# Kernel tuning notes

Hardware: AMD Instinct MI355X
Metric: run time of the kernel (lower is better)

Reference implementation:

```python
import jax, jax.numpy as jnp
import numpy as np

H, W = 1080, 1920
NPART = 25          # BODY_25 joint parts (channel 25 is background)
NLIMB = 26          # 26 PAF limbs -> 52 PAF channels
K = 32              # max peaks kept per joint (static top-k)
MID = 10            # mid_num line samples
THRE1 = 0.1
SIGMA = 3.0
RADIUS = 12         # scipy gaussian_filter: int(truncate*sigma+0.5), truncate=4
# BODY_25 limb sequence (SKEL25DEF.paf_dict), paired with mapIdx [[2k,2k+1]]
LIMBS = np.array([[1,8],[1,2],[1,5],[2,3],[3,4],[5,6],[6,7],[8,9],[9,10],
                  [10,11],[8,12],[12,13],[13,14],[1,0],[0,15],[15,16],[0,17],
                  [0,18],[14,19],[19,20],[14,21],[11,22],[22,23],[11,24],
                  [2,17],[5,18]], dtype=np.int32)


def gaussian_blur(x):
    """Separable gaussian filter, sigma=3, scipy mode='reflect' (= np symmetric). x: [H,W,C]."""
    C = x.shape[-1]
    t = jnp.arange(-RADIUS, RADIUS + 1, dtype=x.dtype)
    k = jnp.exp(-0.5 * (t / SIGMA) ** 2)
    k = k / k.sum()
    dn = ('NHWC', 'HWIO', 'NHWC')
    # vertical pass
    xp = jnp.pad(x, ((RADIUS, RADIUS), (0, 0), (0, 0)), mode='symmetric')[None]
    kh = jnp.tile(k.reshape(-1, 1, 1, 1), (1, 1, 1, C))
    x1 = jax.lax.conv_general_dilated(xp, kh, (1, 1), 'VALID',
                                      dimension_numbers=dn, feature_group_count=C)
    # horizontal pass
    x1 = jnp.pad(x1, ((0, 0), (0, 0), (RADIUS, RADIUS), (0, 0)), mode='symmetric')
    kw = jnp.tile(k.reshape(1, -1, 1, 1), (1, 1, 1, C))
    x2 = jax.lax.conv_general_dilated(x1, kw, (1, 1), 'VALID',
                                      dimension_numbers=dn, feature_group_count=C)
    return x2[0]


def openpose_post(heatmap_avg, paf_avg):
    maps = heatmap_avg[:, :, :NPART]                      # [H,W,25] map_ori per part
    sm = gaussian_blur(maps)                              # one_heatmap per part
    z_row = jnp.zeros((1, W, NPART), sm.dtype)
    z_col = jnp.zeros((H, 1, NPART), sm.dtype)
    m_left = jnp.concatenate([z_row, sm[:-1]], axis=0)
    m_right = jnp.concatenate([sm[1:], z_row], axis=0)
    m_up = jnp.concatenate([z_col, sm[:, :-1]], axis=1)
    m_down = jnp.concatenate([sm[:, 1:], z_col], axis=1)
    peaks_bin = ((sm >= m_left) & (sm >= m_right) & (sm >= m_up)
                 & (sm >= m_down) & (sm > THRE1))
    # static per-part top-K peaks, scored by the ORIGINAL (unblurred) map value
    flat = jnp.where(peaks_bin, maps, -1e9).transpose(2, 0, 1).reshape(NPART, H * W)
    vals, idx = jax.lax.top_k(flat, K)                    # [25,K]
    mask = vals > -1e8
    py = (idx // W).astype(jnp.int32)
    px = (idx % W).astype(jnp.int32)
    peak_x = px.astype(maps.dtype)
    peak_y = py.astype(maps.dtype)
    peak_scores = jnp.where(mask, vals, 0.0)

    limbs = jnp.asarray(LIMBS)
    ax, ay, ma = peak_x[limbs[:, 0]], peak_y[limbs[:, 0]], mask[limbs[:, 0]]  # [26,K]
    bx, by, mb = peak_x[limbs[:, 1]], peak_y[limbs[:, 1]], mask[limbs[:, 1]]
    paf_pairs = jnp.moveaxis(paf_avg.reshape(H, W, NLIMB, 2), 2, 0)           # [26,H,W,2]

    def limb_conn(paf2, ax, ay, bx, by, ma, mb):
        vx = bx[None, :] - ax[:, None]                    # [K,K]
        vy = by[None, :] - ay[:, None]
        norm = jnp.sqrt(vx * vx + vy * vy) + 1e-10
        ux, uy = vx / norm, vy / norm
        t = jnp.linspace(0.0, 1.0, MID, dtype=ax.dtype)   # matches np.linspace(a,b,10)
        sx = jnp.round(ax[:, None, None] + vx[:, :, None] * t).astype(jnp.int32)  # [K,K,MID]
        sy = jnp.round(ay[:, None, None] + vy[:, :, None] * t).astype(jnp.int32)
        pvx = paf2[sy, sx, 0]
        pvy = paf2[sy, sx, 1]
        score = (pvx * ux[:, :, None] + pvy * uy[:, :, None]).mean(-1)
        score = jnp.clip(score, 0.0, 1.0)
        return jnp.where(ma[:, None] & mb[None, :], score, 0.0)

    conn = jax.vmap(limb_conn)(paf_pairs, ax, ay, bx, by, ma, mb)             # [26,K,K]
    return peak_x, peak_y, peak_scores, mask, conn


def setup_inputs() -> dict:
    key = jax.random.key(0)
    k1, k2 = jax.random.split(key)
    heatmap_avg = jax.random.uniform(k1, (H, W, NPART + 1), dtype=jnp.float32)
    paf_avg = jax.random.normal(k2, (H, W, 2 * NLIMB), dtype=jnp.float32) * 0.3
    return {"heatmap_avg": heatmap_avg, "paf_avg": paf_avg}


def reference(heatmap_avg, paf_avg):
    return openpose_post(heatmap_avg, paf_avg)
```

## Files before the change

### kernel.cpp

```cpp
#include <hip/hip_runtime.h>
#include <math.h>
#include <float.h>

#define H 1080
#define W 1920
#define HWSZ (H*W)
#define NPART 25
#define NCH 26
#define NLIMB 26
#define KTOP 32
#define MID 10
#define RAD 12

#define EPS1 4e-6f
#define EPS2 1.5e-7
#define BLCAP (1 << 20)
#define B3CAP 65536
#define NS 16

#define VB 10
#define VXT 16
#define VCHUNK 50
#define TH2 14
#define TW2B 256
#define VTC2 282
#define VTS2 283
#define SMS2 257

#define OFF_PY   800
#define OFF_SC   1600
#define OFF_MK   2400
#define OFF_CONN 3200

__device__ __constant__ int LIMBS_d[NLIMB * 2] = {
    1,8, 1,2, 1,5, 2,3, 3,4, 5,6, 6,7, 8,9, 9,10, 10,11, 8,12, 12,13, 13,14,
    1,0, 0,15, 15,16, 0,17, 0,18, 14,19, 19,20, 14,21, 11,22, 22,23, 11,24, 2,17, 5,18
};

__device__ __forceinline__ int symH(int y) {
    if (y < 0) return -1 - y;
    if (y >= H) return 2 * H - 1 - y;
    return y;
}
__device__ __forceinline__ int symW(int x) {
    if (x < 0) return -1 - x;
    if (x >= W) return 2 * W - 1 - x;
    return x;
}

__global__ void winit_k(double* __restrict__ gw64, float* __restrict__ gw32)
{
    if (threadIdx.x == 0) {
        double wd[25]; double s = 0.0;
        for (int t = 0; t < 25; ++t) {
            double u = (double)(t - 12) / 3.0;
            wd[t] = exp(-0.5 * u * u); s += wd[t];
        }
        for (int t = 0; t < 13; ++t) {
            double w = wd[t] / s;
            gw64[t] = w;
            gw32[t] = (float)w;
        }
    }
}

__global__ __launch_bounds__(416) void vert_k(
    const float* __restrict__ hm, float* __restrict__ vpl,
    const double* __restrict__ gw64)
{
    __shared__ float ldv[VB][26][17];
    const int tid = threadIdx.x;
    const int x0 = blockIdx.x * VXT;
    const int ys = blockIdx.y * VCHUNK;
    const int c  = tid % 26;
    const int xo = tid / 26;
    const int gx = x0 + xo;

    double ws[13];
    #pragma unroll
    for (int t = 0; t < 13; ++t) ws[t] = gw64[t];

    const size_t cstr = (size_t)W * NCH;
    const size_t base = (size_t)gx * NCH + c;
    const bool yint = (ys >= 12) && (ys + 61 < H);

    double win[25];
    if (yint) {
        const float* p0 = hm + (size_t)(ys - 12) * cstr + base;
        #pragma unroll
        for (int k = 0; k < 24; ++k) { win[k] = (double)*p0; p0 += cstr; }
    } else {
        #pragma unroll
        for (int k = 0; k < 24; ++k) {
            int ry = symH(ys - 12 + k);
            win[k] = (double)hm[(size_t)ry * cstr + base];
        }
    }
    win[24] = 0.0;

    const float* pn = hm + (size_t)symH(ys + 12) * cstr + base;

    #pragma unroll 1
    for (int blk = 0; blk < VCHUNK; blk += 25) {
        #pragma unroll
        for (int p = 0; p < 25; ++p) {
            const int yo = blk + p;
            const int y  = ys + yo;
            double nv;
            if (yint) { nv = (double)*pn; pn += cstr; }
            else      { int ry = symH(y + 12); nv = (double)hm[(size_t)ry * cstr + base]; }
            win[(p + 24) % 25] = nv;
            double acc = 0.0;
            #pragma unroll
            for (int t = 0; t < 25; ++t)
                acc = fma(ws[t < 13 ? t : 24 - t], win[(p + t) % 25], acc);
            if (c < 25) ldv[yo % VB][c][xo] = (float)acc;
            if ((yo % VB) == VB - 1) {
                __syncthreads();
                const int c2 = tid >> 4, x2 = tid & 15;
                if (c2 < 25) {
                    const int yb = ys + yo - (VB - 1);
                    #pragma unroll
                    for (int i = 0; i < VB; ++i) {
                        int yr = yb + i;
                        if (yr < H)
                            vpl[(size_t)c2 * HWSZ + (size_t)yr * W + x0 + x2] = ldv[i][c2][x2];
                    }
                }
                __syncthreads();
            }
        }
    }
}

__global__ __launch_bounds__(256) void horiz_nms_k(
    const float* __restrict__ vpl, const float* __restrict__ hm,
    float* __restrict__ cval, int* __restrict__ cidx,
    int* __restrict__ counters, unsigned int* __restrict__ blg,
    const float* __restrict__ gw32, int cap)
{
    __shared__ __align__(16) float ubuf[16 * VTS2];
    float (*vt)[VTS2]  = reinterpret_cast<float(*)[VTS2]>(ubuf);
    float (*smt)[SMS2] = reinterpret_cast<float(*)[SMS2]>(ubuf);
    __shared__ unsigned short cand[TH2 * TW2B];
    __shared__ unsigned int bl[1024];
    __shared__ int lcount, bcount, gbase, gbase2;

    const int tid = threadIdx.x;
    const int r   = tid & 15;
    const int g   = tid >> 4;
    const int ch  = blockIdx.z;
    const int x0  = blockIdx.x * TW2B;
    const int y0  = blockIdx.y * TH2;
    const float* vp = vpl + (size_t)ch * HWSZ;

    if (tid == 0) { lcount = 0; bcount = 0; }
    float w32[13];
    #pragma unroll
    for (int t = 0; t < 13; ++t) w32[t] = gw32[t];

    {
        const int lr  = tid >> 4;
        const int lc0 = tid & 15;
        int gy = y0 - 1 + lr;
        gy = gy < 0 ? 0 : (gy >= H ? H - 1 : gy);
        const float* rowp = vp + (size_t)gy * W;
        const bool xint = (x0 >= 13) && (x0 + (VTC2 - 13) <= W);
        if (xint) {
            const float* p = rowp + (x0 - 13) + lc0;
            #pragma unroll
            for (int j = 0; j < 18; ++j) {
                int cc = lc0 + 16 * j;
                if (cc < VTC2) vt[lr][cc] = p[16 * j];
            }
        } else {
            #pragma unroll
            for (int j = 0; j < 18; ++j) {
                int cc = lc0 + 16 * j;
                if (cc < VTC2) vt[lr][cc] = rowp[symW(x0 - 13 + cc)];
            }
        }
    }
    __syncthreads();

    float xr[42];
    {
        const float* vrow = &vt[r][g * 16];
        #pragma unroll
        for (int t = 0; t < 42; ++t) xr[t] = vrow[t];
    }
    __syncthreads();

    float a[18];
    #pragma unroll
    for (int k = 0; k < 18; ++k) a[k] = 0.f;
    #pragma unroll
    for (int tap = 0; tap < 25; ++tap) {
        const int wi = tap < 13 ? tap : 24 - tap;
        const float wt = w32[wi];
        #pragma unroll
        for (int k = 0; k < 18; ++k)
            a[k] = fmaf(wt, xr[k + tap], a[k]);
    }

    const int gy_r = y0 - 1 + r;
    {
        const bool rowok = (gy_r >= 0 && gy_r < H);
        #pragma unroll
        for (int k = 1; k <= 16; ++k) {
            int j = g * 16 + k - 1;
            int gxj = x0 + j;
            smt[r][j] = (rowok && gxj < W) ? a[k] : 0.f;
        }
    }
    __syncthreads();

    if (r >= 1 && r <= 14 && gy_r < H) {
        const float* up = &smt[r - 1][g * 16];
        const float* dn = &smt[r + 1][g * 16];
        const int ly = r - 1;
        #pragma unroll
        for (int k = 0; k < 16; ++k) {
            int gx = x0 + g * 16 + k;
            if (gx >= W) continue;
            float s  = a[k + 1];
            float lv = (gx == 0) ? 0.f : a[k];
            float rv = (gx + 1 >= W) ? 0.f : a[k + 2];
            float dT = s - 0.1f;
            float d0 = s - up[k];
            float d1 = s - dn[k];
            float d2 = s - lv;
            float d3 = s - rv;
            int flags = (fabsf(dT) <= EPS1 ? 1 : 0)
                      | (fabsf(d0) <= EPS1 ? 2 : 0)
                      | (fabsf(d1) <= EPS1 ? 4 : 0)
                      | (fabsf(d2) <= EPS1 ? 8 : 0)
                      | (fabsf(d3) <= EPS1 ? 16 : 0);
            if (!flags) {
                if (dT > 0.f && d0 >= 0.f && d1 >= 0.f && d2 >= 0.f && d3 >= 0.f) {
                    int pos = atomicAdd(&lcount, 1);
                    cand[pos] = (unsigned short)((ly << 8) | (g * 16 + k));
                }
            } else {
                bool fail = (!(flags & 1)  && dT <= 0.f) ||
                            (!(flags & 2)  && d0 <  0.f) ||
                            (!(flags & 4)  && d1 <  0.f) ||
                            (!(flags & 8)  && d2 <  0.f) ||
                            (!(flags & 16) && d3 <  0.f);
                if (!fail) {
                    unsigned int ent = ((unsigned int)ch << 26) | ((unsigned int)flags << 21)
                                     | (unsigned int)((y0 + ly) * W + gx);
                    int bp = atomicAdd(&bcount, 1);
                    if (bp < 1024) bl[bp] = ent;
                    else {
                        int gp = atomicAdd(&counters[32], 1);
                        if (gp < BLCAP) blg[gp] = ent;
                    }
                }
            }
        }
    }
    __syncthreads();

    if (tid == 0) {
        gbase  = atomicAdd(&counters[ch], lcount);
        int nb = bcount < 1024 ? bcount : 1024;
        gbase2 = atomicAdd(&counters[32], nb);
    }
    __syncthreads();
    int n = lcount, b = gbase;
    for (int i = tid; i < n; i += 256) {
        int p = b + i;
        if (p < cap) {
            int e = cand[i];
            int ly = e >> 8, lx = e & 255;
            int gpix = (y0 + ly) * W + (x0 + lx);
            cval[(size_t)ch * cap + p] = hm[(size_t)gpix * NCH + ch];
            cidx[(size_t)ch * cap + p] = gpix;
        }
    }
    int nb = bcount < 1024 ? bcount : 1024;
    for (int i = tid; i < nb; i += 256) {
        int gp = gbase2 + i;
        if (gp < BLCAP) blg[gp] = bl[i];
    }
}

__device__ __forceinline__ double smh2(const float* __restrict__ vp,
                                       const double* w64s, int y, int x)
{
    int lane = threadIdx.x & 63;
    double term = 0.0;
    if (lane < 25) {
        int cx = symW(x - RAD + lane);
        int wi = lane < 13 ? lane : 24 - lane;
        term = w64s[wi] * (double)vp[(size_t)y * W + cx];
    }
    #pragma unroll
    for (int off = 16; off > 0; off >>= 1)
        term += __shfl_xor(term, off, 64);
    return __shfl(term, 0, 64);
}

__global__ __launch_bounds__(64) void recheck2_k(
    const float* __restrict__ vpl, const float* __restrict__ hm,
    float* __restrict__ cval, int* __restrict__ cidx,
    int* __restrict__ counters, const unsigned int* __restrict__ blg,
    unsigned int* __restrict__ bl3, const double* __restrict__ gw64, int cap)
{
    __shared__ double w64s[13];
    const int tid = threadIdx.x;
    if (tid < 13) w64s[tid] = gw64[tid];
    __syncthreads();

    int total = counters[32];
    if (total > BLCAP) total = BLCAP;
    for (int e = blockIdx.x; e < total; e += gridDim.x) {
        unsigned int ent = blg[e];
        int ch    = (int)(ent >> 26);
        int flags = (int)((ent >> 21) & 31);
        int gpix  = (int)(ent & 0x1FFFFFu);
        int gy = gpix / W, gx = gpix - gy * W;
        const float* vp = vpl + (size_t)ch * HWSZ;

        double sc = smh2(vp, w64s, gy, gx);
        bool dead = false; bool esc = false;
        if (flags & 1) {
            double d = sc - 0.1;
            if (d <= -EPS2) dead = true; else if (d < EPS2) esc = true;
        }
        if (!dead && (flags & 2)) {
            double nv = (gy - 1 >= 0) ? smh2(vp, w64s, gy - 1, gx) : 0.0;
            double d = sc - nv;
            if (d <= -EPS2) dead = true; else if (d < EPS2) esc = true;
        }
        if (!dead && (flags & 4)) {
            double nv = (gy + 1 < H) ? smh2(vp, w64s, gy + 1, gx) : 0.0;
            double d = sc - nv;
            if (d <= -EPS2) dead = true; else if (d < EPS2) esc = true;
        }
        if (!dead && (flags & 8)) {
            double nv = (gx - 1 >= 0) ? smh2(vp, w64s, gy, gx - 1) : 0.0;
            double d = sc - nv;
            if (d <= -EPS2) dead = true; else if (d < EPS2) esc = true;
        }
        if (!dead && (flags & 16)) {
            double nv = (gx + 1 < W) ? smh2(vp, w64s, gy, gx + 1) : 0.0;
            double d = sc - nv;
            if (d <= -EPS2) dead = true; else if (d < EPS2) esc = true;
        }
        if (!dead && tid == 0) {
            if (esc) {
                int p = atomicAdd(&counters[33], 1);
                if (p < B3CAP) bl3[p] = ent;
            } else {
                int p = atomicAdd(&counters[ch], 1);
                if (p < cap) {
                    cval[(size_t)ch * cap + p] = hm[(size_t)gpix * NCH + ch];
                    cidx[(size_t)ch * cap + p] = gpix;
                }
            }
        }
    }
}

__device__ double sm64_eval(const float* __restrict__ hm, int ch,
                            const double* w64s, int y, int x)
{
    int lane = threadIdx.x & 63;
    double colsum = 0.0;
    if (lane < 25) {
        int cx = symW(x - RAD + lane);
        float xv[25];
        #pragma unroll
        for (int t = 0; t < 25; t++) {
            int ry = symH(y - RAD + t);
            xv[t] = hm[((size_t)ry * W + cx) * NCH + ch];
        }
        #pragma unroll
        for (int t = 0; t < 25; t++)
            colsum = fma(w64s[t < 13 ? t : 24 - t], (double)xv[t], colsum);
    }
    double acc = 0.0;
    for (int ci = 0; ci < 25; ci++) {
        double cs = __shfl(colsum, ci, 64);
        acc = fma(w64s[ci < 13 ? ci : 24 - ci], cs, acc);
    }
    return acc;
}

__global__ __launch_bounds__(64) void recheck3_k(
    const float* __restrict__ hm,
    float* __restrict__ cval, int* __restrict__ cidx,
    int* __restrict__ counters, const unsigned int* __restrict__ bl3,
    const double* __restrict__ gw64, int cap)
{
    __shared__ double w64s[13];
    const int tid = threadIdx.x;
    if (tid < 13) w64s[tid] = gw64[tid];
    __syncthreads();

    int total = counters[33];
    if (total > B3CAP) total = B3CAP;
    for (int e = blockIdx.x; e < total; e += gridDim.x) {
        unsigned int ent = bl3[e];
        int ch    = (int)(ent >> 26);
        int flags = (int)((ent >> 21) & 31);
        int gpix  = (int)(ent & 0x1FFFFFu);
        int gy = gpix / W, gx = gpix - gy * W;
        double sc = sm64_eval(hm, ch, w64s, gy, gx);
        bool ok = (flags & 1) ? (sc > 0.1) : true;
        if (ok && (flags & 2))  { double nv = (gy - 1 >= 0) ? sm64_eval(hm, ch, w64s, gy - 1, gx) : 0.0; ok = (sc >= nv); }
        if (ok && (flags & 4))  { double nv = (gy + 1 <  H) ? sm64_eval(hm, ch, w64s, gy + 1, gx) : 0.0; ok = (sc >= nv); }
        if (ok && (flags & 8))  { double nv = (gx - 1 >= 0) ? sm64_eval(hm, ch, w64s, gy, gx - 1) : 0.0; ok = (sc >= nv); }
        if (ok && (flags & 16)) { double nv = (gx + 1 <  W) ? sm64_eval(hm, ch, w64s, gy, gx + 1) : 0.0; ok = (sc >= nv); }
        if (tid == 0 && ok) {
            int p = atomicAdd(&counters[ch], 1);
            if (p < cap) {
                cval[(size_t)ch * cap + p] = hm[(size_t)gpix * NCH + ch];
                cidx[(size_t)ch * cap + p] = gpix;
            }
        }
    }
}

#define TH 32
#define TW 64
#define LR (TH + 2*RAD + 2)
#define LC 90
#define VRR 34
#define VC (TW + 2*RAD + 2)
#define SR 34
#define SC 66
__global__ __launch_bounds__(256) void blur_peaks_gather(
    const float* __restrict__ hm,
    float* __restrict__ cval, int* __restrict__ cidx,
    int* __restrict__ counters, int cap)
{
    __shared__ float  in_t[LR][LC];
    __shared__ double v[VRR][VC];
    __shared__ double smv[SR][SC];
    __shared__ double wgt[2 * RAD + 1];
    __shared__ double wsum;

    const int tid = threadIdx.x;
    const int ch  = blockIdx.x;
    const int x0  = blockIdx.y * TW;
    const int y0  = blockIdx.z * TH;

    if (tid < 2 * RAD + 1) {
        double t = (double)(tid - RAD) / 3.0;
        wgt[tid] = exp(-0.5 * t * t);
    }
    __syncthreads();
    if (tid == 0) {
        double s = 0.0;
        for (int i = 0; i < 2 * RAD + 1; i++) s += wgt[i];
        wsum = s;
    }
    __syncthreads();
    if (tid < 2 * RAD + 1) wgt[tid] /= wsum;

    for (int i = tid; i < LR * LC; i += 256) {
        int r = i / LC, c = i % LC;
        int gy = symH(y0 - RAD - 1 + r);
        int gx = symW(x0 - RAD - 1 + c);
        in_t[r][c] = hm[((size_t)gy * W + gx) * NCH + ch];
    }
    __syncthreads();

    for (int i = tid; i < VRR * VC; i += 256) {
        int r = i / VC, c = i % VC;
        double acc = 0.0;
        #pragma unroll
        for (int t = 0; t < 2 * RAD + 1; t++)
            acc = fma(wgt[t], (double)in_t[r + t][c], acc);
        v[r][c] = acc;
    }
    __syncthreads();

    for (int i = tid; i < SR * SC; i += 256) {
        int r = i / SC, cc = i % SC;
        int gy = y0 - 1 + r;
        int gx = x0 - 1 + cc;
        double acc = 0.0;
        if (gy >= 0 && gy < H && gx >= 0 && gx < W) {
            #pragma unroll
            for (int t = 0; t < 2 * RAD + 1; t++)
                acc = fma(wgt[t], v[r][cc + t], acc);
        }
        smv[r][cc] = acc;
    }
    __syncthreads();

    for (int i = tid; i < TH * TW; i += 256) {
        int ly = i / TW, lx = i % TW;
        int gy = y0 + ly, gx = x0 + lx;
        if (gy >= H || gx >= W) continue;
        double s = smv[ly + 1][lx + 1];
        if (s > 0.1 &&
            s >= smv[ly][lx + 1] && s >= smv[ly + 2][lx + 1] &&
            s >= smv[ly + 1][lx] && s >= smv[ly + 1][lx + 2]) {
            float val = in_t[ly + RAD + 1][lx + RAD + 1];
            int pos = atomicAdd(&counters[ch], 1);
            if (pos < cap) {
                cval[(size_t)ch * cap + pos] = val;
                cidx[(size_t)ch * cap + pos] = gy * W + gx;
            }
        }
    }
}

#define BT 128
__global__ __launch_bounds__(BT) void topk1_kernel(
    const float* __restrict__ cval, const int* __restrict__ cidx,
    const int* __restrict__ counters, int cap,
    unsigned long long* __restrict__ s1)
{
    __shared__ unsigned long long lk[KTOP * BT];
    __shared__ unsigned long long rk[BT];
    __shared__ int rw[BT];
    __shared__ int winner;

    const int tid = threadIdx.x;
    const int sl  = blockIdx.x;
    const int ch  = blockIdx.y;
    int n = counters[ch];
    if (n > cap) n = cap;

    int cnt = 0;
    for (int j = sl * BT + tid; j < n; j += NS * BT) {
        float v = cval[(size_t)ch * cap + j];
        unsigned int u = __float_as_uint(v);
        u = (u & 0x80000000u) ? ~u : (u | 0x80000000u);
        unsigned long long key =
            ((unsigned long long)u << 32) |
            (unsigned int)(0xFFFFFFFFu - (unsigned int)cidx[(size_t)ch * cap + j]);
        if (cnt == KTOP) {
            if (key <= lk[(KTOP - 1) * BT + tid]) continue;
            cnt = KTOP - 1;
        }
        int i = cnt;
        while (i > 0 && key > lk[(i - 1) * BT + tid]) {
            lk[i * BT + tid] = lk[(i - 1) * BT + tid];
            i--;
        }
        lk[i * BT + tid] = key;
        cnt++;
    }
    int cur = 0;
    __syncthreads();

    for (int k = 0; k < KTOP; k++) {
        rk[tid] = (cur < cnt) ? lk[cur * BT + tid] : 0ULL;
        rw[tid] = tid;
        __syncthreads();
        for (int s = BT / 2; s > 0; s >>= 1) {
            if (tid < s) {
                if (rk[tid + s] > rk[tid]) { rk[tid] = rk[tid + s]; rw[tid] = rw[tid + s]; }
            }
            __syncthreads();
        }
        if (tid == 0) {
            winner = rw[0];
            s1[((size_t)ch * NS + sl) * KTOP + k] = rk[0];
        }
        __syncthreads();
        if (tid == winner && cur < cnt) cur++;
        __syncthreads();
    }
}

__global__ __launch_bounds__(BT) void topk2_kernel(
    const unsigned long long* __restrict__ s1,
    const int* __restrict__ counters, int cap, float* __restrict__ out)
{
    __shared__ unsigned long long sk[NS * KTOP];
    const int tid = threadIdx.x;
    const int ch  = blockIdx.x;

    for (int i = tid; i < NS * KTOP; i += BT)
        sk[i] = s1[(size_t)ch * NS * KTOP + i];
    __syncthreads();

    for (int k = 2; k <= NS * KTOP; k <<= 1) {
        for (int j = k >> 1; j > 0; j >>= 1) {
            for (int t = tid; t < NS * KTOP; t += BT) {
                int ixj = t ^ j;
                if (ixj > t) {
                    unsigned long long a = sk[t], b = sk[ixj];
                    bool sw = ((t & k) == 0) ? (a < b) : (a > b);
                    if (sw) { sk[t] = b; sk[ixj] = a; }
                }
            }
            __syncthreads();
        }
    }

    int n = counters[ch];
    if (n > cap) n = cap;
    if (tid < KTOP) {
        unsigned long long bk = sk[tid];
        float px, py, sc, mk;
        if (bk == 0ULL) {
            int fake = tid - n; if (fake < 0) fake = 0;
            px = (float)(fake % W); py = (float)(fake / W); sc = 0.f; mk = 0.f;
        } else {
            unsigned int u = (unsigned int)(bk >> 32);
            unsigned int fb = (u & 0x80000000u) ? (u ^ 0x80000000u) : ~u;
            float v = __uint_as_float(fb);
            int idx = (int)(0xFFFFFFFFu - (unsigned int)(bk & 0xFFFFFFFFu));
            px = (float)(idx % W); py = (float)(idx / W); sc = v; mk = 1.f;
        }
        out[ch * KTOP + tid]          = px;
        out[OFF_PY + ch * KTOP + tid] = py;
        out[OFF_SC + ch * KTOP + tid] = sc;
        out[OFF_MK + ch * KTOP + tid] = mk;
    }
}

__global__ __launch_bounds__(BT) void topk_kernel(
    const float* __restrict__ cval, const int* __restrict__ cidx,
    const int* __restrict__ counters, int cap, float* __restrict__ out)
{
    __shared__ unsigned long long lk[KTOP * BT];
    __shared__ unsigned long long rk[BT];
    __shared__ int rw[BT];
    __shared__ int winner;

    const int tid = threadIdx.x;
    const int ch  = blockIdx.x;
    int n = counters[ch];
    if (n > cap) n = cap;

    int cnt = 0;
    for (int j = tid; j < n; j += BT) {
        float v = cval[(size_t)ch * cap + j];
        unsigned int u = __float_as_uint(v);
        u = (u & 0x80000000u) ? ~u : (u | 0x80000000u);
        unsigned long long key =
            ((unsigned long long)u << 32) |
            (unsigned int)(0xFFFFFFFFu - (unsigned int)cidx[(size_t)ch * cap + j]);
        if (cnt == KTOP) {
            if (key <= lk[(KTOP - 1) * BT + tid]) continue;
            cnt = KTOP - 1;
        }
        int i = cnt;
        while (i > 0 && key > lk[(i - 1) * BT + tid]) {
            lk[i * BT + tid] = lk[(i - 1) * BT + tid];
            i--;
        }
        lk[i * BT + tid] = key;
        cnt++;
    }
    int cur = 0;
    __syncthreads();

    for (int k = 0; k < KTOP; k++) {
        rk[tid] = (cur < cnt) ? lk[cur * BT + tid] : 0ULL;
        rw[tid] = tid;
        __syncthreads();
        for (int s = BT / 2; s > 0; s >>= 1) {
            if (tid < s) {
                if (rk[tid + s] > rk[tid]) { rk[tid] = rk[tid + s]; rw[tid] = rw[tid + s]; }
            }
            __syncthreads();
        }
        if (tid == 0) {
            winner = rw[0];
            unsigned long long bk = rk[0];
            float px, py, sc, mk;
            if (bk == 0ULL) {
                int fake = k - n; if (fake < 0) fake = 0;
                px = (float)(fake % W); py = (float)(fake / W); sc = 0.f; mk = 0.f;
            } else {
                unsigned int u = (unsigned int)(bk >> 32);
                unsigned int fb = (u & 0x80000000u) ? (u ^ 0x80000000u) : ~u;
                float v = __uint_as_float(fb);
                int idx = (int)(0xFFFFFFFFu - (unsigned int)(bk & 0xFFFFFFFFu));
                px = (float)(idx % W); py = (float)(idx / W); sc = v; mk = 1.f;
            }
            out[ch * KTOP + k]          = px;
            out[OFF_PY + ch * KTOP + k] = py;
            out[OFF_SC + ch * KTOP + k] = sc;
            out[OFF_MK + ch * KTOP + k] = mk;
        }
        __syncthreads();
        if (tid == winner && cur < cnt) cur++;
        __syncthreads();
    }
}

__global__ __launch_bounds__(1024) void limbs_kernel(
    const float* __restrict__ pk, const float* __restrict__ paf,
    float* __restrict__ out)
{
    const int l = blockIdx.x;
    const int tid = threadIdx.x;
    const int i = tid >> 5;
    const int j = tid & 31;
    const int A = LIMBS_d[2 * l], B = LIMBS_d[2 * l + 1];

    float ax = pk[A * KTOP + i],          ay = pk[OFF_PY + A * KTOP + i];
    float ma = pk[OFF_MK + A * KTOP + i];
    float bx = pk[B * KTOP + j],          by = pk[OFF_PY + B * KTOP + j];
    float mb = pk[OFF_MK + B * KTOP + j];

    float vx = bx - ax, vy = by - ay;
    float norm = sqrtf(vx * vx + vy * vy) + 1e-10f;
    float ux = vx / norm, uy = vy / norm;

    const float step = 1.0f / 9.0f;
    float sum = 0.f;
    #pragma unroll
    for (int m = 0; m < MID; m++) {
        float t = (float)m * step;
        int sx = (int)rintf(ax + vx * t);
        int sy = (int)rintf(ay + vy * t);
        const float* p = paf + ((size_t)sy * W + sx) * (2 * NLIMB) + 2 * l;
        sum += p[0] * ux + p[1] * uy;
    }
    float score = sum / (float)MID;
    score = score < 0.f ? 0.f : (score > 1.f ? 1.f : score);
    float res = (ma != 0.f && mb != 0.f) ? score : 0.f;
    out[OFF_CONN + l * (KTOP * KTOP) + i * KTOP + j] = res;
}

extern "C" void kernel_launch(void* const* d_in, const int* in_sizes, int n_in,
                              void* d_out, int out_size, void* d_ws, size_t ws_size,
                              hipStream_t stream)
{
    const float* hm  = (const float*)d_in[0];
    const float* paf = (const float*)d_in[1];
    float* out = (float*)d_out;

    const size_t vpl_bytes = (size_t)NPART * HWSZ * sizeof(float);
    const size_t bl_bytes  = (size_t)BLCAP * 4;
    const size_t b3_bytes  = (size_t)B3CAP * 4;
    const size_t s1_bytes  = (size_t)NPART * NS * KTOP * 8;
    const size_t head = 512;

    bool pathA = false;
    int cap = 1;
    if (ws_size > head + vpl_bytes + bl_bytes + b3_bytes + s1_bytes
                 + (size_t)NPART * 8 * 4096 + 1024) {
        size_t avail = ws_size - head - vpl_bytes - bl_bytes - b3_bytes - s1_bytes - 1024;
        long long c = (long long)(avail / ((size_t)NPART * 8));
        cap = c > 65536 ? 65536 : (int)c;
        pathA = true;
    } else {
        size_t avail = ws_size > head ? ws_size - head : 0;
        long long c = (long long)(avail / ((size_t)NPART * 8));
        cap = c > 65536 ? 65536 : (int)c;
        if (cap < 1) cap = 1;
    }

    int*    counters = (int*)d_ws;
    double* gw64 = (double*)((char*)d_ws + 256);
    float*  gw32 = (float*)((char*)d_ws + 384);
    float* cval = (float*)((char*)d_ws + head);
    int*   cidx = (int*)(cval + (size_t)NPART * cap);
    unsigned long long* s1 = (unsigned long long*)(cidx + (size_t)NPART * cap);
    unsigned int* blg = (unsigned int*)(s1 + (pathA ? (size_t)NPART * NS * KTOP : 0));
    unsigned int* bl3 = blg + (pathA ? (size_t)BLCAP : 0);
    float* vpl = (float*)(bl3 + (pathA ? (size_t)B3CAP : 0));
    vpl = (float*)(((uintptr_t)vpl + 255) & ~(uintptr_t)255);

    hipMemsetAsync(d_ws, 0, 256, stream);

    if (pathA) {
        winit_k<<<1, 64, 0, stream>>>(gw64, gw32);
        dim3 g1(W / VXT, (H + VCHUNK - 1) / VCHUNK);
        vert_k<<<g1, 416, 0, stream>>>(hm, vpl, gw64);
        dim3 g2((W + TW2B - 1) / TW2B, (H + TH2 - 1) / TH2, NPART);
        horiz_nms_k<<<g2, 256, 0, stream>>>(vpl, hm, cval, cidx, counters, blg, gw32, cap);
        recheck2_k<<<2048, 64, 0, stream>>>(vpl, hm, cval, cidx, counters, blg, bl3, gw64, cap);
        recheck3_k<<<256, 64, 0, stream>>>(hm, cval, cidx, counters, bl3, gw64, cap);
        dim3 gt(NS, NPART);
        topk1_kernel<<<gt, BT, 0, stream>>>(cval, cidx, counters, cap, s1);
        topk2_kernel<<<NPART, BT, 0, stream>>>(s1, counters, cap, out);
    } else {
        dim3 gA(NPART, (W + TW - 1) / TW, (H + TH - 1) / TH);
        blur_peaks_gather<<<gA, 256, 0, stream>>>(hm, cval, cidx, counters, cap);
        topk_kernel<<<NPART, BT, 0, stream>>>(cval, cidx, counters, cap, out);
    }
    limbs_kernel<<<NLIMB, 1024, 0, stream>>>(out, paf, out);
}
```

Baseline: 534.8 us.

## Enlarge blur tiles, stream horizontal taps, and merge recheck kernels

Doubles the vertical chunk height and moves the horizontal NMS kernel to 512-thread blocks covering 30 output rows, which cuts redundant halo rows and block count. The horizontal convolution now reads each shared value once and applies it to every tap it contributes to, instead of first copying 42 values into registers. The per-block candidate buffer is capped, with overflow written straight to global memory. The third recheck kernel is folded into the second, so escalated pixels are re-evaluated in double precision inline rather than through a separate list and launch, which adds divergence inside the merged kernel.

```diff
diff --git a/kernel.cpp b/kernel.cpp
--- a/kernel.cpp
+++ b/kernel.cpp
@@ -15,17 +15,17 @@
 #define EPS1 4e-6f
 #define EPS2 1.5e-7
 #define BLCAP (1 << 20)
-#define B3CAP 65536
 #define NS 16
 
 #define VB 10
 #define VXT 16
-#define VCHUNK 50
-#define TH2 14
+#define VCHUNK 100
+#define TH2S 30
 #define TW2B 256
 #define VTC2 282
 #define VTS2 283
 #define SMS2 257
+#define CANDC 2048
 
 #define OFF_PY   800
 #define OFF_SC   1600
@@ -82,7 +82,7 @@
 
     const size_t cstr = (size_t)W * NCH;
     const size_t base = (size_t)gx * NCH + c;
-    const bool yint = (ys >= 12) && (ys + 61 < H);
+    const bool yint = (ys >= 12) && (ys + VCHUNK + 11 < H);
 
     double win[25];
     if (yint) {
@@ -133,25 +133,25 @@
     }
 }
 
-__global__ __launch_bounds__(256) void horiz_nms_k(
+__global__ __launch_bounds__(512) void horiz_nms_k(
     const float* __restrict__ vpl, const float* __restrict__ hm,
     float* __restrict__ cval, int* __restrict__ cidx,
     int* __restrict__ counters, unsigned int* __restrict__ blg,
     const float* __restrict__ gw32, int cap)
 {
-    __shared__ __align__(16) float ubuf[16 * VTS2];
+    __shared__ __align__(16) float ubuf[32 * VTS2];
     float (*vt)[VTS2]  = reinterpret_cast<float(*)[VTS2]>(ubuf);
     float (*smt)[SMS2] = reinterpret_cast<float(*)[SMS2]>(ubuf);
-    __shared__ unsigned short cand[TH2 * TW2B];
+    __shared__ unsigned short cand[CANDC];
     __shared__ unsigned int bl[1024];
     __shared__ int lcount, bcount, gbase, gbase2;
 
     const int tid = threadIdx.x;
-    const int r   = tid & 15;
-    const int g   = tid >> 4;
+    const int r   = tid & 31;
+    const int g   = tid >> 5;
     const int ch  = blockIdx.z;
     const int x0  = blockIdx.x * TW2B;
-    const int y0  = blockIdx.y * TH2;
+    const int y0  = blockIdx.y * TH2S;
     const float* vp = vpl + (size_t)ch * HWSZ;
 
     if (tid == 0) { lcount = 0; bcount = 0; }
@@ -183,25 +183,23 @@
     }
     __syncthreads();
 
-    float xr[42];
-    {
-        const float* vrow = &vt[r][g * 16];
-        #pragma unroll
-        for (int t = 0; t < 42; ++t) xr[t] = vrow[t];
-    }
-    __syncthreads();
-
     float a[18];
     #pragma unroll
     for (int k = 0; k < 18; ++k) a[k] = 0.f;
-    #pragma unroll
-    for (int tap = 0; tap < 25; ++tap) {
-        const int wi = tap < 13 ? tap : 24 - tap;
-        const float wt = w32[wi];
-        #pragma unroll
-        for (int k = 0; k < 18; ++k)
-            a[k] = fmaf(wt, xr[k + tap], a[k]);
-    }
+    {
+        const float* vrow = &vt[r][g * 16];
+        #pragma unroll
+        for (int t = 0; t < 42; ++t) {
+            float x = vrow[t];
+            #pragma unroll
+            for (int k = 0; k < 18; ++k)
+                if (t >= k && t < k + 25) {
+                    int wi = t - k; wi = wi < 13 ? wi : 24 - wi;
+                    a[k] = fmaf(w32[wi], x, a[k]);
+                }
+        }
+    }
+    __syncthreads();
 
     const int gy_r = y0 - 1 + r;
     {
@@ -215,7 +213,7 @@
     }
     __syncthreads();
 
-    if (r >= 1 && r <= 14 && gy_r < H) {
+    if (r >= 1 && r <= TH2S && gy_r < H) {
         const float* up = &smt[r - 1][g * 16];
         const float* dn = &smt[r + 1][g * 16];
         const int ly = r - 1;
@@ -239,7 +237,15 @@
             if (!flags) {
                 if (dT > 0.f && d0 >= 0.f && d1 >= 0.f && d2 >= 0.f && d3 >= 0.f) {
                     int pos = atomicAdd(&lcount, 1);
-                    cand[pos] = (unsigned short)((ly << 8) | (g * 16 + k));
+                    int gpix = (y0 + ly) * W + gx;
+                    if (pos < CANDC) cand[pos] = (unsigned short)((ly << 8) | (g * 16 + k));
+                    else {
+                        int p = atomicAdd(&counters[ch], 1);
+                        if (p < cap) {
+                            cval[(size_t)ch * cap + p] = hm[(size_t)gpix * NCH + ch];
+                            cidx[(size_t)ch * cap + p] = gpix;
+                        }
+                    }
                 }
             } else {
                 bool fail = (!(flags & 1)  && dT <= 0.f) ||
@@ -263,13 +269,15 @@
     __syncthreads();
 
     if (tid == 0) {
-        gbase  = atomicAdd(&counters[ch], lcount);
+        int nl = lcount < CANDC ? lcount : CANDC;
+        gbase  = atomicAdd(&counters[ch], nl);
         int nb = bcount < 1024 ? bcount : 1024;
         gbase2 = atomicAdd(&counters[32], nb);
     }
     __syncthreads();
-    int n = lcount, b = gbase;
-    for (int i = tid; i < n; i += 256) {
+    int n = lcount < CANDC ? lcount : CANDC;
+    int b = gbase;
+    for (int i = tid; i < n; i += 512) {
         int p = b + i;
         if (p < cap) {
             int e = cand[i];
@@ -280,7 +288,7 @@
         }
     }
     int nb = bcount < 1024 ? bcount : 1024;
-    for (int i = tid; i < nb; i += 256) {
+    for (int i = tid; i < nb; i += 512) {
         int gp = gbase2 + i;
         if (gp < BLCAP) blg[gp] = bl[i];
     }
@@ -302,11 +310,36 @@
     return __shfl(term, 0, 64);
 }
 
-__global__ __launch_bounds__(64) void recheck2_k(
+__device__ double sm64_eval(const float* __restrict__ hm, int ch,
+                            const double* w64s, int y, int x)
+{
+    int lane = threadIdx.x & 63;
+    double colsum = 0.0;
+    if (lane < 25) {
+        int cx = symW(x - RAD + lane);
+        float xv[25];
+        #pragma unroll
+        for (int t = 0; t < 25; t++) {
+            int ry = symH(y - RAD + t);
+            xv[t] = hm[((size_t)ry * W + cx) * NCH + ch];
+        }
+        #pragma unroll
+        for (int t = 0; t < 25; t++)
+            colsum = fma(w64s[t < 13 ? t : 24 - t], (double)xv[t], colsum);
+    }
+    double acc = 0.0;
+    for (int ci = 0; ci < 25; ci++) {
+        double cs = __shfl(colsum, ci, 64);
+        acc = fma(w64s[ci < 13 ? ci : 24 - ci], cs, acc);
+    }
+    return acc;
+}
+
+__global__ __launch_bounds__(64) void recheck_k(
     const float* __restrict__ vpl, const float* __restrict__ hm,
     float* __restrict__ cval, int* __restrict__ cidx,
     int* __restrict__ counters, const unsigned int* __restrict__ blg,
-    unsigned int* __restrict__ bl3, const double* __restrict__ gw64, int cap)
+    const double* __restrict__ gw64, int cap)
 {
     __shared__ double w64s[13];
     const int tid = threadIdx.x;
@@ -349,72 +382,18 @@
             double d = sc - nv;
             if (d <= -EPS2) dead = true; else if (d < EPS2) esc = true;
         }
-        if (!dead && tid == 0) {
-            if (esc) {
-                int p = atomicAdd(&counters[33], 1);
-                if (p < B3CAP) bl3[p] = ent;
-            } else {
-                int p = atomicAdd(&counters[ch], 1);
-                if (p < cap) {
-                    cval[(size_t)ch * cap + p] = hm[(size_t)gpix * NCH + ch];
-                    cidx[(size_t)ch * cap + p] = gpix;
-                }
-            }
-        }
-    }
-}
-
-__device__ double sm64_eval(const float* __restrict__ hm, int ch,
-                            const double* w64s, int y, int x)
-{
-    int lane = threadIdx.x & 63;
-    double colsum = 0.0;
-    if (lane < 25) {
-        int cx = symW(x - RAD + lane);
-        float xv[25];
-        #pragma unroll
-        for (int t = 0; t < 25; t++) {
-            int ry = symH(y - RAD + t);
-            xv[t] = hm[((size_t)ry * W + cx) * NCH + ch];
-        }
-        #pragma unroll
-        for (int t = 0; t < 25; t++)
-            colsum = fma(w64s[t < 13 ? t : 24 - t], (double)xv[t], colsum);
-    }
-    double acc = 0.0;
-    for (int ci = 0; ci < 25; ci++) {
-        double cs = __shfl(colsum, ci, 64);
-        acc = fma(w64s[ci < 13 ? ci : 24 - ci], cs, acc);
-    }
-    return acc;
-}
-
-__global__ __launch_bounds__(64) void recheck3_k(
-    const float* __restrict__ hm,
-    float* __restrict__ cval, int* __restrict__ cidx,
-    int* __restrict__ counters, const unsigned int* __restrict__ bl3,
-    const double* __restrict__ gw64, int cap)
-{
-    __shared__ double w64s[13];
-    const int tid = threadIdx.x;
-    if (tid < 13) w64s[tid] = gw64[tid];
-    __syncthreads();
-
-    int total = counters[33];
-    if (total > B3CAP) total = B3CAP;
-    for (int e = blockIdx.x; e < total; e += gridDim.x) {
-        unsigned int ent = bl3[e];
-        int ch    = (int)(ent >> 26);
-        int flags = (int)((ent >> 21) & 31);
-        int gpix  = (int)(ent & 0x1FFFFFu);
-        int gy = gpix / W, gx = gpix - gy * W;
-        double sc = sm64_eval(hm, ch, w64s, gy, gx);
-        bool ok = (flags & 1) ? (sc > 0.1) : true;
-        if (ok && (flags & 2))  { double nv = (gy - 1 >= 0) ? sm64_eval(hm, ch, w64s, gy - 1, gx) : 0.0; ok = (sc >= nv); }
-        if (ok && (flags & 4))  { double nv = (gy + 1 <  H) ? sm64_eval(hm, ch, w64s, gy + 1, gx) : 0.0; ok = (sc >= nv); }
-        if (ok && (flags & 8))  { double nv = (gx - 1 >= 0) ? sm64_eval(hm, ch, w64s, gy, gx - 1) : 0.0; ok = (sc >= nv); }
-        if (ok && (flags & 16)) { double nv = (gx + 1 <  W) ? sm64_eval(hm, ch, w64s, gy, gx + 1) : 0.0; ok = (sc >= nv); }
-        if (tid == 0 && ok) {
+        bool accept = false;
+        if (!dead && !esc) accept = true;
+        else if (!dead && esc) {
+            double sE = sm64_eval(hm, ch, w64s, gy, gx);
+            bool ok = (flags & 1) ? (sE > 0.1) : true;
+            if (ok && (flags & 2))  { double nv = (gy - 1 >= 0) ? sm64_eval(hm, ch, w64s, gy - 1, gx) : 0.0; ok = (sE >= nv); }
+            if (ok && (flags & 4))  { double nv = (gy + 1 <  H) ? sm64_eval(hm, ch, w64s, gy + 1, gx) : 0.0; ok = (sE >= nv); }
+            if (ok && (flags & 8))  { double nv = (gx - 1 >= 0) ? sm64_eval(hm, ch, w64s, gy, gx - 1) : 0.0; ok = (sE >= nv); }
+            if (ok && (flags & 16)) { double nv = (gx + 1 <  W) ? sm64_eval(hm, ch, w64s, gy, gx + 1) : 0.0; ok = (sE >= nv); }
+            accept = ok;
+        }
+        if (accept && tid == 0) {
             int p = atomicAdd(&counters[ch], 1);
             if (p < cap) {
                 cval[(size_t)ch * cap + p] = hm[(size_t)gpix * NCH + ch];
@@ -736,15 +715,14 @@
 
     const size_t vpl_bytes = (size_t)NPART * HWSZ * sizeof(float);
     const size_t bl_bytes  = (size_t)BLCAP * 4;
-    const size_t b3_bytes  = (size_t)B3CAP * 4;
     const size_t s1_bytes  = (size_t)NPART * NS * KTOP * 8;
     const size_t head = 512;
 
     bool pathA = false;
     int cap = 1;
-    if (ws_size > head + vpl_bytes + bl_bytes + b3_bytes + s1_bytes
+    if (ws_size > head + vpl_bytes + bl_bytes + s1_bytes
                  + (size_t)NPART * 8 * 4096 + 1024) {
-        size_t avail = ws_size - head - vpl_bytes - bl_bytes - b3_bytes - s1_bytes - 1024;
+        size_t avail = ws_size - head - vpl_bytes - bl_bytes - s1_bytes - 1024;
         long long c = (long long)(avail / ((size_t)NPART * 8));
         cap = c > 65536 ? 65536 : (int)c;
         pathA = true;
@@ -762,8 +740,7 @@
     int*   cidx = (int*)(cval + (size_t)NPART * cap);
     unsigned long long* s1 = (unsigned long long*)(cidx + (size_t)NPART * cap);
     unsigned int* blg = (unsigned int*)(s1 + (pathA ? (size_t)NPART * NS * KTOP : 0));
-    unsigned int* bl3 = blg + (pathA ? (size_t)BLCAP : 0);
-    float* vpl = (float*)(bl3 + (pathA ? (size_t)B3CAP : 0));
+    float* vpl = (float*)(blg + (pathA ? (size_t)BLCAP : 0));
     vpl = (float*)(((uintptr_t)vpl + 255) & ~(uintptr_t)255);
 
     hipMemsetAsync(d_ws, 0, 256, stream);
@@ -772,10 +749,9 @@
         winit_k<<<1, 64, 0, stream>>>(gw64, gw32);
         dim3 g1(W / VXT, (H + VCHUNK - 1) / VCHUNK);
         vert_k<<<g1, 416, 0, stream>>>(hm, vpl, gw64);
-        dim3 g2((W + TW2B - 1) / TW2B, (H + TH2 - 1) / TH2, NPART);
-        horiz_nms_k<<<g2, 256, 0, stream>>>(vpl, hm, cval, cidx, counters, blg, gw32, cap);
-        recheck2_k<<<2048, 64, 0, stream>>>(vpl, hm, cval, cidx, counters, blg, bl3, gw64, cap);
-        recheck3_k<<<256, 64, 0, stream>>>(hm, cval, cidx, counters, bl3, gw64, cap);
+        dim3 g2((W + TW2B - 1) / TW2B, H / TH2S, NPART);
+        horiz_nms_k<<<g2, 512, 0, stream>>>(vpl, hm, cval, cidx, counters, blg, gw32, cap);
+        recheck_k<<<2048, 64, 0, stream>>>(vpl, hm, cval, cidx, counters, blg, gw64, cap);
         dim3 gt(NS, NPART);
         topk1_kernel<<<gt, BT, 0, stream>>>(cval, cidx, counters, cap, s1);
         topk2_kernel<<<NPART, BT, 0, stream>>>(s1, counters, cap, out);
```

Result: faster. 442.3 us (median of 2 runs) (-17.3%).
